# Performance work log

Measured on AMD Instinct MI355X. Metric: run time of the kernel, lower is better.

## Reference

```python
import jax, jax.numpy as jnp
import numpy as np

EPS = 1e-7  # K.epsilon()


def setup_inputs() -> dict:
    key = jax.random.key(0)
    k1, k2, k3 = jax.random.split(key, 3)
    B, H, W, Cin, Cout, KH, KW = 8, 128, 128, 256, 256, 3, 3
    x = jax.random.normal(k1, (B, H, W, Cin), dtype=jnp.float32)
    style = jax.random.normal(k2, (B, Cin), dtype=jnp.float32)
    # he_uniform-ish scale for the kernel
    fan_in = KH * KW * Cin
    limit = np.sqrt(6.0 / fan_in)
    kernel = jax.random.uniform(k3, (KH, KW, Cin, Cout), dtype=jnp.float32,
                                minval=-limit, maxval=limit)
    return {"x": x, "style": style, "kernel": kernel}


def reference(x, style, kernel):
    # Demodulation factor: rsqrt(sum_{kh,kw,cin} (kernel * style)^2 + eps), shape (B, Cout).
    # Equivalent to the original's broadcast-then-reduce, computed without
    # materializing the (B,kh,kw,Cin,Cout) modulated weight tensor.
    k2 = jnp.sum(jnp.square(kernel), axis=(0, 1))          # (Cin, Cout)
    ssq = jnp.einsum('io,bi->bo', k2, jnp.square(style))   # (B, Cout)
    demod = jax.lax.rsqrt(ssq + EPS)                       # (B, Cout)

    # Modulate input per-sample, then shared-weight conv (same padding, stride 1).
    xm = x * style[:, None, None, :]                       # (B,H,W,Cin)
    y = jax.lax.conv_general_dilated(
        xm, kernel,
        window_strides=(1, 1), padding='SAME',
        dimension_numbers=('NHWC', 'HWIO', 'NHWC'))
    return y * demod[:, None, None, :]
```

## Files before the change

kernel.cpp:

```cpp
#include <hip/hip_runtime.h>
#include <hip/hip_bf16.h>
#include <stdint.h>

typedef short short8 __attribute__((ext_vector_type(8)));
typedef float f32x4 __attribute__((ext_vector_type(4)));

#define KKTOT 2304
#define PXS   40

__device__ __forceinline__ short f2bf(float f) {
    __hip_bfloat16 h = __float2bfloat16(f);
    return __builtin_bit_cast(short, h);
}

__global__ void prep_k2(const float* __restrict__ kern, float* __restrict__ K2)
{
    const int ci = blockIdx.x, co = threadIdx.x;
    float acc = 0.f;
#pragma unroll
    for (int p = 0; p < 9; ++p) {
        float w = kern[(p * 256 + ci) * 256 + co];
        acc += w * w;
    }
    K2[ci * 256 + co] = acc;
}

__global__ void prep_demod(const float* __restrict__ style,
                           const float* __restrict__ K2,
                           float* __restrict__ demod)
{
    const int b = blockIdx.x, co = threadIdx.x;
    __shared__ float s2[256];
    float s = style[b * 256 + co];
    s2[co] = s * s;
    __syncthreads();
    float acc = 0.f;
#pragma unroll 8
    for (int ci = 0; ci < 256; ++ci)
        acc += s2[ci] * K2[ci * 256 + co];
    demod[b * 256 + co] = 1.0f / sqrtf(acc + 1e-7f);
}

__global__ void prep_kt(const float* __restrict__ kern,
                        __hip_bfloat16* __restrict__ kT)
{
    __shared__ float tile[64][65];
    const int t   = threadIdx.x;
    const int k0  = blockIdx.x << 6;
    const int c0  = blockIdx.y << 6;
    const int col = t & 63;
    const int rb  = (t >> 6) << 4;
#pragma unroll
    for (int r = 0; r < 16; ++r) {
        int kl = rb + r;
        tile[kl][col] = kern[(size_t)(k0 + kl) * 256 + c0 + col];
    }
    __syncthreads();
#pragma unroll
    for (int r = 0; r < 16; ++r) {
        int co = rb + r;
        kT[(size_t)(c0 + co) * KKTOT + k0 + col] = __float2bfloat16(tile[col][co]);
    }
}

__global__ __launch_bounds__(256) void conv_mfma(
    const float* __restrict__ x,
    const __hip_bfloat16* __restrict__ kt,
    const float* __restrict__ style,
    const float* __restrict__ demod,
    float* __restrict__ out)
{
    __shared__ __align__(16) __hip_bfloat16 Xs[130 * PXS];
    __shared__ __align__(16) __hip_bfloat16 Bs[3 * 128 * PXS];
    __shared__ float Ss[256];
    __shared__ float Ds[128];

    const int t    = threadIdx.x;
    const int bid  = blockIdx.x;
    const int L    = ((bid & 7) << 8) | (bid >> 3);
    const int n0   = (L & 1) << 7;
    const int bh   = L >> 1;
    const int b    = bh >> 7, h = bh & 127;
    const int wave = t >> 6, lane = t & 63;
    const int wr   = (wave >> 1) << 6;
    const int wc   = (wave & 1) << 6;
    const int l15  = lane & 15, lk = lane >> 4;
    const int mA   = t >> 2;
    const int koff = (t & 3) << 3;

    if (t < 128) {
        ((float2*)Ss)[t] = ((const float2*)(style + b * 256))[t];
        Ds[t] = demod[b * 256 + n0 + t];
    }
    if (t < 32) {
        Xs[t]             = __float2bfloat16(0.f);
        Xs[129 * PXS + t] = __float2bfloat16(0.f);
    }

    f32x4 acc[4][4] = {};

    for (int sl = 0; sl < 24; ++sl) {
        const int h2 = h + (sl >> 3) - 1;
        if ((unsigned)h2 >= 128u) continue;
        const int ci0     = (sl & 7) << 5;
        const int posbase = (sl >> 3) * 3;

        __syncthreads();

        const size_t rowbase = (size_t)(b * 128 + h2) * 128;
        const float* ga = x + (rowbase + mA)      * 256 + ci0 + koff;
        const float* gb = x + (rowbase + mA + 64) * 256 + ci0 + koff;
        float4 xa0 = *(const float4*)ga,       xa1 = *(const float4*)(ga + 4);
        float4 xb0 = *(const float4*)gb,       xb1 = *(const float4*)(gb + 4);
        float4 s0  = *(const float4*)&Ss[ci0 + koff];
        float4 s1  = *(const float4*)&Ss[ci0 + koff + 4];
        short8 ma, mb;
#pragma unroll
        for (int jj = 0; jj < 4; ++jj) {
            ma[jj]     = f2bf((&xa0.x)[jj] * (&s0.x)[jj]);
            ma[jj + 4] = f2bf((&xa1.x)[jj] * (&s1.x)[jj]);
            mb[jj]     = f2bf((&xb0.x)[jj] * (&s0.x)[jj]);
            mb[jj + 4] = f2bf((&xb1.x)[jj] * (&s1.x)[jj]);
        }
        *(short8*)&Xs[(mA + 1)  * PXS + koff] = ma;
        *(short8*)&Xs[(mA + 65) * PXS + koff] = mb;

        const __hip_bfloat16* gw =
            kt + (size_t)(n0 + mA) * KKTOT + posbase * 256 + ci0 + koff;
#pragma unroll
        for (int tp = 0; tp < 3; ++tp) {
            short8 w0 = *(const short8*)(gw + tp * 256);
            short8 w1 = *(const short8*)(gw + tp * 256 + 64 * KKTOT);
            *(short8*)&Bs[tp * (128 * PXS) + mA * PXS + koff]        = w0;
            *(short8*)&Bs[tp * (128 * PXS) + (mA + 64) * PXS + koff] = w1;
        }
        __syncthreads();

#pragma unroll
        for (int tp = 0; tp < 3; ++tp) {
            short8 af[4], bfr[4];
#pragma unroll
            for (int i = 0; i < 4; ++i)
                af[i] = *(const short8*)&Xs[(wr + i * 16 + l15 + tp) * PXS + lk * 8];
#pragma unroll
            for (int j = 0; j < 4; ++j)
                bfr[j] = *(const short8*)&Bs[tp * (128 * PXS) + (wc + j * 16 + l15) * PXS + lk * 8];
#pragma unroll
            for (int i = 0; i < 4; ++i)
#pragma unroll
                for (int j = 0; j < 4; ++j)
                    acc[i][j] = __builtin_amdgcn_mfma_f32_16x16x32_bf16(
                        af[i], bfr[j], acc[i][j], 0, 0, 0);
        }
    }

    float dj[4];
#pragma unroll
    for (int j = 0; j < 4; ++j) dj[j] = Ds[wc + j * 16 + l15];
    const size_t obase = (size_t)(b * 128 + h) * 128 * 256 + n0;
#pragma unroll
    for (int i = 0; i < 4; ++i) {
#pragma unroll
        for (int j = 0; j < 4; ++j) {
            const int n = wc + j * 16 + l15;
#pragma unroll
            for (int r = 0; r < 4; ++r) {
                const int m = wr + i * 16 + lk * 4 + r;
                out[obase + (size_t)m * 256 + n] = acc[i][j][r] * dj[j];
            }
        }
    }
}

extern "C" void kernel_launch(void* const* d_in, const int* in_sizes, int n_in,
                              void* d_out, int out_size, void* d_ws, size_t ws_size,
                              hipStream_t stream)
{
    const float* x     = (const float*)d_in[0];
    const float* style = (const float*)d_in[1];
    const float* kern  = (const float*)d_in[2];
    float* out = (float*)d_out;

    char*  ws    = (char*)d_ws;
    float* demod = (float*)ws;
    float* K2    = (float*)(ws + 8192);
    __hip_bfloat16* kT = (__hip_bfloat16*)(ws + 270336);

    prep_k2   <<<256, 256, 0, stream>>>(kern, K2);
    prep_demod<<<8,   256, 0, stream>>>(style, K2, demod);
    prep_kt   <<<dim3(36, 4), 256, 0, stream>>>(kern, kT);
    conv_mfma <<<2048, 256, 0, stream>>>(x, kT, style, demod, out);
}
```

Before: 361.9 us.

## Compute two output rows per block to reuse weight tiles across rows

```diff
diff --git a/kernel.cpp b/kernel.cpp
--- a/kernel.cpp
+++ b/kernel.cpp
@@ -63,110 +63,123 @@
     }
 }
 
-__global__ __launch_bounds__(256) void conv_mfma(
+__global__ __launch_bounds__(256, 2) void conv_mfma(
     const float* __restrict__ x,
     const __hip_bfloat16* __restrict__ kt,
     const float* __restrict__ style,
     const float* __restrict__ demod,
     float* __restrict__ out)
 {
-    __shared__ __align__(16) __hip_bfloat16 Xs[130 * PXS];
-    __shared__ __align__(16) __hip_bfloat16 Bs[3 * 128 * PXS];
+    __shared__ __align__(16) __hip_bfloat16 Xs[2][130 * PXS];
+    __shared__ __align__(16) __hip_bfloat16 Bs[3][128 * PXS];
     __shared__ float Ss[256];
     __shared__ float Ds[128];
 
-    const int t    = threadIdx.x;
-    const int bid  = blockIdx.x;
-    const int L    = ((bid & 7) << 8) | (bid >> 3);
-    const int n0   = (L & 1) << 7;
-    const int bh   = L >> 1;
-    const int b    = bh >> 7, h = bh & 127;
+    const int t   = threadIdx.x;
+    const int bid = blockIdx.x;
+    const int vid = ((bid & 7) << 7) | (bid >> 3);
+    const int n0  = (vid & 1) << 7;
+    const int b   = (vid >> 1) & 7;
+    const int h0  = (vid >> 4) << 1;
+
     const int wave = t >> 6, lane = t & 63;
-    const int wr   = (wave >> 1) << 6;
-    const int wc   = (wave & 1) << 6;
+    const int j    = wave >> 1;
+    const int ch   = wave & 1;
     const int l15  = lane & 15, lk = lane >> 4;
-    const int mA   = t >> 2;
-    const int koff = (t & 3) << 3;
+
+    const int p    = t >> 1;
+    const int ck   = (t & 1) << 4;
+    const int mB   = t >> 2;
+    const int kofB = (t & 3) << 3;
 
     if (t < 128) {
         ((float2*)Ss)[t] = ((const float2*)(style + b * 256))[t];
         Ds[t] = demod[b * 256 + n0 + t];
     }
-    if (t < 32) {
-        Xs[t]             = __float2bfloat16(0.f);
-        Xs[129 * PXS + t] = __float2bfloat16(0.f);
-    }
-
-    f32x4 acc[4][4] = {};
+    if (t < 64) {
+        int jh = t >> 5, i2 = t & 31;
+        Xs[jh][i2]             = __float2bfloat16(0.f);
+        Xs[jh][129 * PXS + i2] = __float2bfloat16(0.f);
+    }
+
+    f32x4 acc[8][4] = {};
 
     for (int sl = 0; sl < 24; ++sl) {
-        const int h2 = h + (sl >> 3) - 1;
-        if ((unsigned)h2 >= 128u) continue;
+        const int dh      = (sl >> 3) - 1;
         const int ci0     = (sl & 7) << 5;
         const int posbase = (sl >> 3) * 3;
 
         __syncthreads();
 
-        const size_t rowbase = (size_t)(b * 128 + h2) * 128;
-        const float* ga = x + (rowbase + mA)      * 256 + ci0 + koff;
-        const float* gb = x + (rowbase + mA + 64) * 256 + ci0 + koff;
-        float4 xa0 = *(const float4*)ga,       xa1 = *(const float4*)(ga + 4);
-        float4 xb0 = *(const float4*)gb,       xb1 = *(const float4*)(gb + 4);
-        float4 s0  = *(const float4*)&Ss[ci0 + koff];
-        float4 s1  = *(const float4*)&Ss[ci0 + koff + 4];
-        short8 ma, mb;
-#pragma unroll
-        for (int jj = 0; jj < 4; ++jj) {
-            ma[jj]     = f2bf((&xa0.x)[jj] * (&s0.x)[jj]);
-            ma[jj + 4] = f2bf((&xa1.x)[jj] * (&s1.x)[jj]);
-            mb[jj]     = f2bf((&xb0.x)[jj] * (&s0.x)[jj]);
-            mb[jj + 4] = f2bf((&xb1.x)[jj] * (&s1.x)[jj]);
-        }
-        *(short8*)&Xs[(mA + 1)  * PXS + koff] = ma;
-        *(short8*)&Xs[(mA + 65) * PXS + koff] = mb;
+        float4 sv0 = *(const float4*)&Ss[ci0 + ck];
+        float4 sv1 = *(const float4*)&Ss[ci0 + ck + 4];
+        float4 sv2 = *(const float4*)&Ss[ci0 + ck + 8];
+        float4 sv3 = *(const float4*)&Ss[ci0 + ck + 12];
+#pragma unroll
+        for (int jj2 = 0; jj2 < 2; ++jj2) {
+            const int r = h0 + jj2 + dh;
+            short8 m0, m1;
+            if ((unsigned)r < 128u) {
+                const float* g = x + ((size_t)((b * 128 + r) * 128 + p)) * 256 + ci0 + ck;
+                float4 v0 = *(const float4*)g;
+                float4 v1 = *(const float4*)(g + 4);
+                float4 v2 = *(const float4*)(g + 8);
+                float4 v3 = *(const float4*)(g + 12);
+#pragma unroll
+                for (int q = 0; q < 4; ++q) {
+                    m0[q]     = f2bf((&v0.x)[q] * (&sv0.x)[q]);
+                    m0[q + 4] = f2bf((&v1.x)[q] * (&sv1.x)[q]);
+                    m1[q]     = f2bf((&v2.x)[q] * (&sv2.x)[q]);
+                    m1[q + 4] = f2bf((&v3.x)[q] * (&sv3.x)[q]);
+                }
+            } else {
+                m0 = short8{}; m1 = short8{};
+            }
+            *(short8*)&Xs[jj2][(p + 1) * PXS + ck]     = m0;
+            *(short8*)&Xs[jj2][(p + 1) * PXS + ck + 8] = m1;
+        }
 
         const __hip_bfloat16* gw =
-            kt + (size_t)(n0 + mA) * KKTOT + posbase * 256 + ci0 + koff;
+            kt + (size_t)(n0 + mB) * KKTOT + posbase * 256 + ci0 + kofB;
 #pragma unroll
         for (int tp = 0; tp < 3; ++tp) {
             short8 w0 = *(const short8*)(gw + tp * 256);
             short8 w1 = *(const short8*)(gw + tp * 256 + 64 * KKTOT);
-            *(short8*)&Bs[tp * (128 * PXS) + mA * PXS + koff]        = w0;
-            *(short8*)&Bs[tp * (128 * PXS) + (mA + 64) * PXS + koff] = w1;
+            *(short8*)&Bs[tp][mB * PXS + kofB]        = w0;
+            *(short8*)&Bs[tp][(mB + 64) * PXS + kofB] = w1;
         }
         __syncthreads();
 
 #pragma unroll
         for (int tp = 0; tp < 3; ++tp) {
-            short8 af[4], bfr[4];
-#pragma unroll
-            for (int i = 0; i < 4; ++i)
-                af[i] = *(const short8*)&Xs[(wr + i * 16 + l15 + tp) * PXS + lk * 8];
-#pragma unroll
-            for (int j = 0; j < 4; ++j)
-                bfr[j] = *(const short8*)&Bs[tp * (128 * PXS) + (wc + j * 16 + l15) * PXS + lk * 8];
-#pragma unroll
-            for (int i = 0; i < 4; ++i)
-#pragma unroll
-                for (int j = 0; j < 4; ++j)
-                    acc[i][j] = __builtin_amdgcn_mfma_f32_16x16x32_bf16(
-                        af[i], bfr[j], acc[i][j], 0, 0, 0);
+            short8 bf[4];
+#pragma unroll
+            for (int jj = 0; jj < 4; ++jj)
+                bf[jj] = *(const short8*)&Bs[tp][(ch * 64 + jj * 16 + l15) * PXS + lk * 8];
+#pragma unroll
+            for (int i = 0; i < 8; ++i) {
+                short8 af = *(const short8*)&Xs[j][(i * 16 + l15 + tp) * PXS + lk * 8];
+#pragma unroll
+                for (int jj = 0; jj < 4; ++jj)
+                    acc[i][jj] = __builtin_amdgcn_mfma_f32_16x16x32_bf16(
+                        af, bf[jj], acc[i][jj], 0, 0, 0);
+            }
         }
     }
 
     float dj[4];
 #pragma unroll
-    for (int j = 0; j < 4; ++j) dj[j] = Ds[wc + j * 16 + l15];
-    const size_t obase = (size_t)(b * 128 + h) * 128 * 256 + n0;
-#pragma unroll
-    for (int i = 0; i < 4; ++i) {
-#pragma unroll
-        for (int j = 0; j < 4; ++j) {
-            const int n = wc + j * 16 + l15;
+    for (int jj = 0; jj < 4; ++jj) dj[jj] = Ds[ch * 64 + jj * 16 + l15];
+    const size_t obase = ((size_t)(b * 128 + h0 + j) * 128) * 256 + n0;
+#pragma unroll
+    for (int i = 0; i < 8; ++i) {
+#pragma unroll
+        for (int jj = 0; jj < 4; ++jj) {
+            const int n = ch * 64 + jj * 16 + l15;
 #pragma unroll
             for (int r = 0; r < 4; ++r) {
-                const int m = wr + i * 16 + lk * 4 + r;
-                out[obase + (size_t)m * 256 + n] = acc[i][j][r] * dj[j];
+                const int m = i * 16 + lk * 4 + r;
+                out[obase + (size_t)m * 256 + n] = acc[i][jj][r] * dj[jj];
             }
         }
     }
@@ -189,5 +202,5 @@
     prep_k2   <<<256, 256, 0, stream>>>(kern, K2);
     prep_demod<<<8,   256, 0, stream>>>(style, K2, demod);
     prep_kt   <<<dim3(36, 4), 256, 0, stream>>>(kern, kT);
-    conv_mfma <<<2048, 256, 0, stream>>>(x, kT, style, demod, out);
-}
+    conv_mfma <<<1024, 256, 0, stream>>>(x, kT, style, demod, out);
+}
```

Result: slower. 370.7 us (+2.4%).
